# Optimization experiments

Hardware: AMD Instinct MI355X
Metric: run time of the kernel (lower is better)

Reference implementation:

```python
import jax, jax.numpy as jnp
import numpy as np

B, C, H, W = 16, 64, 64, 64
K_CLUST, KS, OUT, RANK, MLP = 16, 3, 64, 8, 32
F = C * KS * KS  # 576


def setup_inputs() -> dict:
    key = jax.random.key(0)
    ks = jax.random.split(key, 14)
    rn = lambda k, shp, s=0.05: (jax.random.normal(k, shp, jnp.float32) * s)
    return {
        "x": jax.random.normal(ks[0], (B, C, H, W), jnp.float32),
        "labels": jax.random.randint(ks[1], (B, H, W), 0, K_CLUST),
        "lr_w1": rn(ks[2], (F, MLP)), "lr_b1": rn(ks[3], (MLP,)),
        "lr_w2": rn(ks[4], (MLP, MLP)), "lr_b2": rn(ks[5], (MLP,)),
        "lr_w3": rn(ks[6], (MLP, RANK)), "lr_b3": rn(ks[7], (RANK,)),
        "base_kernels": rn(ks[8], (RANK, F, OUT), 0.1),
        "bw1": rn(ks[9], (F, MLP)), "bb1": rn(ks[10], (MLP,)),
        "bw2": rn(ks[11], (MLP, OUT)), "bb2": rn(ks[12], (OUT,)),
    }


def _extract_patches(x):
    # torch nn.Unfold(kernel=3, padding=1) layout: features ordered (C, kh, kw)
    b, c, h, w = x.shape
    xp = jnp.pad(x, ((0, 0), (0, 0), (1, 1), (1, 1)))
    p = jnp.stack([xp[:, :, i:i + h, j:j + w] for i in range(KS) for j in range(KS)], axis=2)  # [B,C,9,H,W]
    return p.reshape(b, c * KS * KS, h * w).transpose(0, 2, 1)  # [B, HW, F]


def reference(x, labels, lr_w1, lr_b1, lr_w2, lr_b2, lr_w3, lr_b3,
              base_kernels, bw1, bb1, bw2, bb2):
    b, c, h, w = x.shape
    patches = _extract_patches(x)                              # [B, HW, F]
    lab = labels.reshape(b, -1)                                # [B, HW]
    onehot = jax.nn.one_hot(lab, K_CLUST, dtype=patches.dtype) # [B, HW, K]
    counts = onehot.sum(axis=1)                                # [B, K]
    centers = jnp.einsum('bnk,bnf->bkf', onehot, patches) / (counts[:, :, None] + 1e-6)

    hdn = jax.nn.relu(centers @ lr_w1 + lr_b1)
    hdn = jax.nn.relu(hdn @ lr_w2 + lr_b2)
    lowrank = hdn @ lr_w3 + lr_b3                              # [B, K, R]
    bias = jax.nn.relu(centers @ bw1 + bb1) @ bw2 + bb2        # [B, K, O]

    kernels = jnp.einsum('bkr,rfo->bkfo', lowrank, base_kernels)   # [B, K, F, O]
    scores = jnp.einsum('bnf,bkfo->bnko', patches, kernels)        # [B, HW, K, O]
    out = jnp.einsum('bnko,bnk->bno', scores, onehot)
    out = out + jnp.einsum('bko,bnk->bno', bias, onehot)           # per-pixel cluster bias
    return out.reshape(b, h, w, OUT).transpose(0, 3, 1, 2)         # [B, O, H, W]
```

## Files before the change

### kernel.cpp

```cpp
#include <hip/hip_runtime.h>
#include <stdint.h>
#include <stddef.h>

#define NB   16
#define NC   64
#define NH   64
#define NW   64
#define KC   16
#define NOUT 64
#define NRANK 8
#define NMLP 32
#define NF   576
#define NPIX 4096
#define XH   66
#define OROWS 8192

typedef short s16x8 __attribute__((ext_vector_type(8)));
typedef short s16x4 __attribute__((ext_vector_type(4)));
typedef float f32x4 __attribute__((ext_vector_type(4)));

__device__ __forceinline__ unsigned short f2bf(float x) {
    union { float f; uint32_t u; } v; v.f = x;
    uint32_t r = v.u + 0x7FFFu + ((v.u >> 16) & 1u);
    return (unsigned short)(r >> 16);
}
__device__ __forceinline__ float bf2f(unsigned short u) {
    union { uint32_t u; float f; } v; v.u = ((uint32_t)u) << 16;
    return v.f;
}

extern "C" __global__ __launch_bounds__(256)
void k_prep_all(const float* __restrict__ x, const float* __restrict__ basek,
                unsigned short* __restrict__ xcl, unsigned short* __restrict__ basekF)
{
    __shared__ float tile[64 * 65];
    const int blk0 = blockIdx.x;
    const int tid = threadIdx.x;
    if (blk0 < XH * 16) {
        const int b = blk0 & 15, yy = blk0 >> 4;
        unsigned short* dst = xcl + ((size_t)(b * XH + yy) * XH) * 64;
        if (yy == 0 || yy == XH - 1) {
            for (int e = tid; e < XH * 64; e += 256) dst[e] = 0;
            return;
        }
        const int y = yy - 1;
        const float* src = x + (size_t)b * NC * (NH * NW) + y * NW;
        #pragma unroll
        for (int rr = 0; rr < 16; ++rr) {
            int c = rr * 4 + (tid >> 6);
            int xx = tid & 63;
            tile[c * 65 + xx] = src[(size_t)c * (NH * NW) + xx];
        }
        __syncthreads();
        for (int ee = tid; ee < 528; ee += 256) {
            int xx = ee >> 3;
            int c0 = (ee & 7) * 8;
            s16x8 v;
            #pragma unroll
            for (int j = 0; j < 8; ++j) {
                float f = (xx == 0 || xx == XH - 1) ? 0.f : tile[(c0 + j) * 65 + (xx - 1)];
                v[j] = (short)f2bf(f);
            }
            *reinterpret_cast<s16x8*>(dst + ee * 8) = v;
        }
    } else {
        const int blk = blk0 - XH * 16;
        const int ks = blk >> 2, wv = blk & 3;
        unsigned short outv[16];
        #pragma unroll
        for (int i = 0; i < 16; ++i) {
            int e = tid * 16 + i;
            int r = e >> 9;
            int lane = (e >> 3) & 63;
            int j = e & 7;
            int col = wv * 16 + (lane & 15);
            int fp = (lane >> 4) * 8 + ks * 32 + j;
            int tap = fp >> 6, c = fp & 63;
            outv[i] = f2bf(basek[((size_t)r * NF + c * 9 + tap) * NOUT + col]);
        }
        unsigned short* dst = basekF + (size_t)blk * 4096 + tid * 16;
        #pragma unroll
        for (int i = 0; i < 16; ++i) dst[i] = outv[i];
    }
}

extern "C" __global__ __launch_bounds__(1024, 1)
void k_cm(const unsigned short* __restrict__ xcl, const int* __restrict__ labels,
          const float* __restrict__ lw1, const float* __restrict__ lb1,
          const float* __restrict__ lw2, const float* __restrict__ lb2,
          const float* __restrict__ lw3, const float* __restrict__ lb3,
          const float* __restrict__ bw1, const float* __restrict__ bb1,
          const float* __restrict__ bw2, const float* __restrict__ bb2,
          const unsigned short* __restrict__ basekF,
          unsigned short* __restrict__ slotmap, unsigned short* __restrict__ outc)
{
    extern __shared__ __align__(16) char smem[];
    unsigned short* list = (unsigned short*)smem;
    int*   wcnt  = (int*)(smem + 8192);
    float* wsum  = (float*)(smem + 8256);
    float* cbuf  = (float*)(smem + 45120);
    float* p1    = (float*)(smem + 47424);
    float* pb    = (float*)(smem + 48448);
    float* h1    = (float*)(smem + 49472);
    float* h2    = (float*)(smem + 49600);
    float* hb    = (float*)(smem + 49728);
    float* lrs   = (float*)(smem + 49856);
    unsigned short* Wl = (unsigned short*)(smem + 51200);
    float* biasl = (float*)(smem + 157696);

    const int bk = blockIdx.x;
    const int b = bk & 15, k = bk >> 4;
    const int tid = threadIdx.x;
    const int lane = tid & 63, wv = tid >> 6;
    const int st = tid & 255, sg = tid >> 8;
    const int* lab = labels + b * NPIX;

    if (tid == 0) wcnt[0] = 0;
    __syncthreads();
    {
        const int n0 = tid, n1 = 1024 + tid, n2 = 2048 + tid, n3 = 3072 + tid;
        const int l0 = lab[n0], l1 = lab[n1], l2 = lab[n2], l3 = lab[n3];
        const bool q0 = (l0 == k), q1 = (l1 == k), q2 = (l2 == k), q3 = (l3 == k);
        const unsigned long long m0 = __ballot(q0), m1 = __ballot(q1),
                                 m2 = __ballot(q2), m3 = __ballot(q3);
        const int c0 = __popcll(m0), c1 = __popcll(m1),
                  c2 = __popcll(m2), c3 = __popcll(m3);
        int base = 0;
        if (lane == 0)
            base = __hip_atomic_fetch_add(&wcnt[0], c0 + c1 + c2 + c3,
                                          __ATOMIC_RELAXED, __HIP_MEMORY_SCOPE_WORKGROUP);
        base = __shfl(base, 0);
        const unsigned long long lt = (1ull << lane) - 1ull;
        if (q0) { int s = base + __popcll(m0 & lt);
                  list[s] = (unsigned short)n0; slotmap[b * NPIX + n0] = (unsigned short)s; }
        base += c0;
        if (q1) { int s = base + __popcll(m1 & lt);
                  list[s] = (unsigned short)n1; slotmap[b * NPIX + n1] = (unsigned short)s; }
        base += c1;
        if (q2) { int s = base + __popcll(m2 & lt);
                  list[s] = (unsigned short)n2; slotmap[b * NPIX + n2] = (unsigned short)s; }
        base += c2;
        if (q3) { int s = base + __popcll(m3 & lt);
                  list[s] = (unsigned short)n3; slotmap[b * NPIX + n3] = (unsigned short)s; }
    }
    __syncthreads();
    const int cnt = wcnt[0];

    float s00 = 0.f, s01 = 0.f, s02 = 0.f,
          s10 = 0.f, s11 = 0.f, s12 = 0.f,
          s20 = 0.f, s21 = 0.f, s22 = 0.f;
    const unsigned short* xb0 = xcl + (size_t)b * (XH * XH * 64) + lane;
    #pragma unroll 4
    for (int i = wv; i < cnt; i += 16) {
        int n = list[i];
        const unsigned short* p0 = xb0 + (((n >> 6) * XH) + (n & 63)) * 64;
        s00 += bf2f(p0[0]);
        s01 += bf2f(p0[64]);
        s02 += bf2f(p0[128]);
        const unsigned short* prow1 = p0 + XH * 64;
        s10 += bf2f(prow1[0]);
        s11 += bf2f(prow1[64]);
        s12 += bf2f(prow1[128]);
        const unsigned short* prow2 = p0 + 2 * XH * 64;
        s20 += bf2f(prow2[0]);
        s21 += bf2f(prow2[64]);
        s22 += bf2f(prow2[128]);
    }
    {
        float* wrow = wsum + wv * 576 + lane;
        wrow[0 * 64] = s00; wrow[1 * 64] = s01; wrow[2 * 64] = s02;
        wrow[3 * 64] = s10; wrow[4 * 64] = s11; wrow[5 * 64] = s12;
        wrow[6 * 64] = s20; wrow[7 * 64] = s21; wrow[8 * 64] = s22;
    }
    __syncthreads();

    const float inv = 1.f / ((float)cnt + 1e-6f);
    if (tid < NF) {
        int tap = tid >> 6, c = tid & 63;
        float s = 0.f;
        #pragma unroll
        for (int w = 0; w < 16; ++w) s += wsum[w * 576 + tap * 64 + c];
        cbuf[c * 9 + tap] = s * inv;
    }
    __syncthreads();

    if (tid < 256) {
        const int j = tid & 31, ch = tid >> 5;
        float a1 = 0.f, a2 = 0.f;
        for (int i = 0; i < 72; ++i) {
            int f = ch * 72 + i;
            float cv = cbuf[f];
            a1 += cv * lw1[f * NMLP + j];
            a2 += cv * bw1[f * NMLP + j];
        }
        p1[ch * NMLP + j] = a1; pb[ch * NMLP + j] = a2;
    }
    __syncthreads();
    if (tid < NMLP) {
        float a = lb1[tid];
        for (int i = 0; i < 8; ++i) a += p1[i * NMLP + tid];
        h1[tid] = fmaxf(a, 0.f);
    } else if (tid < 2 * NMLP) {
        int j = tid - NMLP;
        float a = bb1[j];
        for (int i = 0; i < 8; ++i) a += pb[i * NMLP + j];
        hb[j] = fmaxf(a, 0.f);
    }
    __syncthreads();
    if (tid < NMLP) {
        float a = lb2[tid];
        for (int i = 0; i < NMLP; ++i) a += h1[i] * lw2[i * NMLP + tid];
        h2[tid] = fmaxf(a, 0.f);
    } else if (tid >= 64 && tid < 128) {
        int o = tid - 64;
        float a = bb2[o];
        for (int i = 0; i < NMLP; ++i) a += hb[i] * bw2[i * NOUT + o];
        biasl[o] = a;
    }
    __syncthreads();
    if (tid < NRANK) {
        float a = lb3[tid];
        for (int i = 0; i < NMLP; ++i) a += h2[i] * lw3[i * NRANK + tid];
        lrs[tid] = a;
    }
    __syncthreads();

    {
        float l8[NRANK];
        #pragma unroll
        for (int r = 0; r < NRANK; ++r) l8[r] = lrs[r];
        #pragma unroll 2
        for (int q = 0; q < 5; ++q) {
            int m = q * 1024 + tid;
            if (m < 4608) {
                int ks = m >> 8, t = m & 255;
                const unsigned short* src = basekF
                    + ((size_t)(ks * 4 + (t >> 6)) * 8) * 512 + (t & 63) * 8;
                float w[8] = {0.f, 0.f, 0.f, 0.f, 0.f, 0.f, 0.f, 0.f};
                #pragma unroll
                for (int r = 0; r < NRANK; ++r) {
                    s16x8 bv = *reinterpret_cast<const s16x8*>(src + r * 512);
                    #pragma unroll
                    for (int j = 0; j < 8; ++j)
                        w[j] += l8[r] * bf2f((unsigned short)bv[j]);
                }
                s16x8 f;
                #pragma unroll
                for (int j = 0; j < 8; ++j) f[j] = (short)f2bf(w[j]);
                *reinterpret_cast<s16x8*>(Wl + m * 8) = f;
            }
        }
    }
    __syncthreads();

    s16x8 bfr[18];
    #pragma unroll
    for (int ks = 0; ks < 18; ++ks)
        bfr[ks] = *reinterpret_cast<const s16x8*>(Wl + ks * 2048 + st * 8);
    __syncthreads();

    {
        const int wv4 = (tid >> 6) & 3;
        const int quad = lane >> 4, l16 = lane & 15;
        unsigned short* albuf = (unsigned short*)(smem + 8192 + sg * 37376);
        const int col = wv4 * 16 + l16;
        const float bb = biasl[col];
        const unsigned short* xb = xcl + (size_t)b * (XH * XH * 64);
        const int p = st >> 3, part = st & 7;
        const int ntile = (cnt + 31) >> 5;
        const int niter = (ntile + 3) >> 2;
        unsigned short* ob = outc + (size_t)b * (OROWS * 64);

        #pragma unroll 1
        for (int it = 0; it < niter; ++it) {
            const int t = it * 4 + sg;
            const bool live = (t < ntile);
            if (live) {
                int slot = (t << 5) + p;
                int n = (slot < cnt) ? (int)list[slot] : 0;
                const unsigned short* xrow =
                    xb + (((n >> 6) * XH) + (n & 63)) * 64 + part * 8;
                unsigned short* arow = albuf + p * 584 + part * 8;
                #pragma unroll
                for (int tap = 0; tap < 9; ++tap) {
                    int dy = tap / 3, dx = tap - dy * 3;
                    *reinterpret_cast<s16x8*>(arow + tap * 64) =
                        *reinterpret_cast<const s16x8*>(xrow + (dy * XH + dx) * 64);
                }
            }
            __syncthreads();
            if (live) {
                f32x4 acc0 = {0.f, 0.f, 0.f, 0.f}, acc1 = {0.f, 0.f, 0.f, 0.f};
                const unsigned short* ar0 = albuf + l16 * 584 + quad * 8;
                const unsigned short* ar1 = ar0 + 16 * 584;
                #pragma unroll
                for (int ks = 0; ks < 18; ++ks) {
                    s16x8 a0 = *reinterpret_cast<const s16x8*>(ar0 + ks * 32);
                    s16x8 a1 = *reinterpret_cast<const s16x8*>(ar1 + ks * 32);
                    acc0 = __builtin_amdgcn_mfma_f32_16x16x32_bf16(a0, bfr[ks], acc0, 0, 0, 0);
                    acc1 = __builtin_amdgcn_mfma_f32_16x16x32_bf16(a1, bfr[ks], acc1, 0, 0, 0);
                }
                #pragma unroll
                for (int r = 0; r < 4; ++r) {
                    int s0 = (t << 5) + quad * 4 + r;
                    if (s0 < cnt)
                        ob[(size_t)(s0 * 16 + k) * 64 + col] = f2bf(acc0[r] + bb);
                    int s1 = s0 + 16;
                    if (s1 < cnt)
                        ob[(size_t)(s1 * 16 + k) * 64 + col] = f2bf(acc1[r] + bb);
                }
            }
            __syncthreads();
        }
    }
}

extern "C" __global__ __launch_bounds__(256)
void k_scatter(const int* __restrict__ labels, const unsigned short* __restrict__ slotmap,
               const unsigned short* __restrict__ outc, float* __restrict__ out)
{
    const int blk = blockIdx.x;
    const int b = blk & 15, chunk = (blk >> 4) & 15, q = blk >> 8;
    const int tid = threadIdx.x;
    __shared__ int sptr[256];
    __shared__ unsigned short tt[256 * 20];
    const int n0 = chunk * 256;
    {
        int n = n0 + tid;
        sptr[tid] = (int)slotmap[b * NPIX + n] * 16 + labels[b * NPIX + n];
    }
    __syncthreads();
    #pragma unroll
    for (int e0 = 0; e0 < 2; ++e0) {
        int e = e0 * 256 + tid;
        int pix = e >> 1, part = e & 1;
        s16x8 vv = *reinterpret_cast<const s16x8*>(
            outc + ((size_t)b * (OROWS * 64)) + (size_t)sptr[pix] * 64 + q * 16 + part * 8);
        s16x4 lo = {vv[0], vv[1], vv[2], vv[3]};
        s16x4 hi = {vv[4], vv[5], vv[6], vv[7]};
        *reinterpret_cast<s16x4*>(tt + pix * 20 + part * 8) = lo;
        *reinterpret_cast<s16x4*>(tt + pix * 20 + part * 8 + 4) = hi;
    }
    __syncthreads();
    float* ob = out + ((size_t)(b * NOUT + q * 16)) * NPIX + n0;
    #pragma unroll
    for (int oo = 0; oo < 16; ++oo)
        ob[(size_t)oo * NPIX + tid] = bf2f(tt[tid * 20 + oo]);
}

extern "C" void kernel_launch(void* const* d_in, const int* in_sizes, int n_in,
                              void* d_out, int out_size, void* d_ws, size_t ws_size,
                              hipStream_t stream)
{
    const float* x      = (const float*)d_in[0];
    const int*   labels = (const int*)d_in[1];
    const float* lw1    = (const float*)d_in[2];
    const float* lb1    = (const float*)d_in[3];
    const float* lw2    = (const float*)d_in[4];
    const float* lb2    = (const float*)d_in[5];
    const float* lw3    = (const float*)d_in[6];
    const float* lb3    = (const float*)d_in[7];
    const float* basek  = (const float*)d_in[8];
    const float* bw1    = (const float*)d_in[9];
    const float* bb1    = (const float*)d_in[10];
    const float* bw2    = (const float*)d_in[11];
    const float* bb2    = (const float*)d_in[12];
    float* out = (float*)d_out;

    char* ws = (char*)d_ws;
    unsigned short* basekF  = (unsigned short*)(ws);
    unsigned short* slotmap = (unsigned short*)(ws + 589824);
    unsigned short* xcl     = (unsigned short*)(ws + 720896);
    unsigned short* outc    = (unsigned short*)(ws + 9641984);

    k_prep_all<<<XH * 16 + 72, 256, 0, stream>>>(x, basek, xcl, basekF);
    k_cm<<<256, 1024, 157952, stream>>>(xcl, labels, lw1, lb1, lw2, lb2, lw3, lb3,
                                        bw1, bb1, bw2, bb2, basekF, slotmap, outc);
    k_scatter<<<1024, 256, 0, stream>>>(labels, slotmap, outc, out);
}
```

Measured before the change: 124.4 us.

## Prefetch next tile's patch rows into registers during MFMA; widen MLP reduction

The main gather/MFMA loop now issues the global loads for the next iteration's nine 3x3 patch taps into registers right after the barrier, so their latency overlaps the current tile's MFMA work. The loaded values are stored to LDS at the start of the following iteration. Separately, the first MLP layer's partial dot products are spread across all 1024 threads (32 chunks of 18 features) instead of 256 threads, with p1/pb moved into the Wl region to fit the larger partial buffers. This costs extra VGPRs for the prefetch registers and relies on the Wl region being free before Wl is written.

Result: slower. 130.4 us (+4.9%).

```diff
diff --git a/kernel.cpp b/kernel.cpp
--- a/kernel.cpp
+++ b/kernel.cpp
@@ -99,12 +99,12 @@
     int*   wcnt  = (int*)(smem + 8192);
     float* wsum  = (float*)(smem + 8256);
     float* cbuf  = (float*)(smem + 45120);
-    float* p1    = (float*)(smem + 47424);
-    float* pb    = (float*)(smem + 48448);
     float* h1    = (float*)(smem + 49472);
     float* h2    = (float*)(smem + 49600);
     float* hb    = (float*)(smem + 49728);
     float* lrs   = (float*)(smem + 49856);
+    float* p1    = (float*)(smem + 51200);
+    float* pb    = (float*)(smem + 55296);
     unsigned short* Wl = (unsigned short*)(smem + 51200);
     float* biasl = (float*)(smem + 157696);
 
@@ -184,11 +184,12 @@
     }
     __syncthreads();
 
-    if (tid < 256) {
+    {
         const int j = tid & 31, ch = tid >> 5;
         float a1 = 0.f, a2 = 0.f;
-        for (int i = 0; i < 72; ++i) {
-            int f = ch * 72 + i;
+        #pragma unroll
+        for (int i = 0; i < 18; ++i) {
+            int f = ch * 18 + i;
             float cv = cbuf[f];
             a1 += cv * lw1[f * NMLP + j];
             a2 += cv * bw1[f * NMLP + j];
@@ -198,12 +199,14 @@
     __syncthreads();
     if (tid < NMLP) {
         float a = lb1[tid];
-        for (int i = 0; i < 8; ++i) a += p1[i * NMLP + tid];
+        #pragma unroll
+        for (int i = 0; i < 32; ++i) a += p1[i * NMLP + tid];
         h1[tid] = fmaxf(a, 0.f);
     } else if (tid < 2 * NMLP) {
         int j = tid - NMLP;
         float a = bb1[j];
-        for (int i = 0; i < 8; ++i) a += pb[i * NMLP + j];
+        #pragma unroll
+        for (int i = 0; i < 32; ++i) a += pb[i * NMLP + j];
         hb[j] = fmaxf(a, 0.f);
     }
     __syncthreads();
@@ -270,25 +273,42 @@
         const int ntile = (cnt + 31) >> 5;
         const int niter = (ntile + 3) >> 2;
         unsigned short* ob = outc + (size_t)b * (OROWS * 64);
-
+        unsigned short* arow = albuf + p * 584 + part * 8;
+
+        s16x8 t0_, t1_, t2_, t3_, t4_, t5_, t6_, t7_, t8_;
+        #define ISSUE(ITER) do { \
+            int slot_ = (((ITER) * 4 + sg) << 5) + p; \
+            int n_ = (slot_ < cnt) ? (int)list[slot_] : 0; \
+            const unsigned short* xr_ = xb + (((n_ >> 6) * XH) + (n_ & 63)) * 64 + part * 8; \
+            t0_ = *reinterpret_cast<const s16x8*>(xr_ + (0 * XH + 0) * 64); \
+            t1_ = *reinterpret_cast<const s16x8*>(xr_ + (0 * XH + 1) * 64); \
+            t2_ = *reinterpret_cast<const s16x8*>(xr_ + (0 * XH + 2) * 64); \
+            t3_ = *reinterpret_cast<const s16x8*>(xr_ + (1 * XH + 0) * 64); \
+            t4_ = *reinterpret_cast<const s16x8*>(xr_ + (1 * XH + 1) * 64); \
+            t5_ = *reinterpret_cast<const s16x8*>(xr_ + (1 * XH + 2) * 64); \
+            t6_ = *reinterpret_cast<const s16x8*>(xr_ + (2 * XH + 0) * 64); \
+            t7_ = *reinterpret_cast<const s16x8*>(xr_ + (2 * XH + 1) * 64); \
+            t8_ = *reinterpret_cast<const s16x8*>(xr_ + (2 * XH + 2) * 64); \
+        } while (0)
+
+        ISSUE(0);
         #pragma unroll 1
         for (int it = 0; it < niter; ++it) {
             const int t = it * 4 + sg;
             const bool live = (t < ntile);
             if (live) {
-                int slot = (t << 5) + p;
-                int n = (slot < cnt) ? (int)list[slot] : 0;
-                const unsigned short* xrow =
-                    xb + (((n >> 6) * XH) + (n & 63)) * 64 + part * 8;
-                unsigned short* arow = albuf + p * 584 + part * 8;
-                #pragma unroll
-                for (int tap = 0; tap < 9; ++tap) {
-                    int dy = tap / 3, dx = tap - dy * 3;
-                    *reinterpret_cast<s16x8*>(arow + tap * 64) =
-                        *reinterpret_cast<const s16x8*>(xrow + (dy * XH + dx) * 64);
-                }
+                *reinterpret_cast<s16x8*>(arow + 0 * 64) = t0_;
+                *reinterpret_cast<s16x8*>(arow + 1 * 64) = t1_;
+                *reinterpret_cast<s16x8*>(arow + 2 * 64) = t2_;
+                *reinterpret_cast<s16x8*>(arow + 3 * 64) = t3_;
+                *reinterpret_cast<s16x8*>(arow + 4 * 64) = t4_;
+                *reinterpret_cast<s16x8*>(arow + 5 * 64) = t5_;
+                *reinterpret_cast<s16x8*>(arow + 6 * 64) = t6_;
+                *reinterpret_cast<s16x8*>(arow + 7 * 64) = t7_;
+                *reinterpret_cast<s16x8*>(arow + 8 * 64) = t8_;
             }
             __syncthreads();
+            if (it + 1 < niter) ISSUE(it + 1);
             if (live) {
                 f32x4 acc0 = {0.f, 0.f, 0.f, 0.f}, acc1 = {0.f, 0.f, 0.f, 0.f};
                 const unsigned short* ar0 = albuf + l16 * 584 + quad * 8;
@@ -312,6 +332,7 @@
             }
             __syncthreads();
         }
+        #undef ISSUE
     }
 }
 
```
